# Optimization experiments

Hardware: AMD Instinct MI355X
Metric: run time of the kernel (lower is better)

Reference implementation:

```python
import jax, jax.numpy as jnp
import numpy as np

N_NODES = 50000
N_EDGES = 500000
D_NODE = 128
D_EDGE = 128
HIDDEN = 64


def setup_inputs() -> dict:
    key = jax.random.key(0)
    k = jax.random.split(key, 8)
    x = jax.random.normal(k[0], (N_NODES, D_NODE), dtype=jnp.float32)
    edge_index = jax.random.randint(k[1], (2, N_EDGES), 0, N_NODES, dtype=jnp.int64)
    e = jax.random.normal(k[2], (N_EDGES, D_EDGE), dtype=jnp.float32)
    d_in = 2 * D_NODE + D_EDGE
    # Kaiming-uniform-ish init like torch Linear
    W1 = jax.random.uniform(k[3], (d_in, HIDDEN), jnp.float32, -1.0, 1.0) / np.sqrt(d_in)
    b1 = jax.random.uniform(k[4], (HIDDEN,), jnp.float32, -1.0, 1.0) / np.sqrt(d_in)
    W2 = jax.random.uniform(k[5], (HIDDEN, D_EDGE), jnp.float32, -1.0, 1.0) / np.sqrt(HIDDEN)
    b2 = jax.random.uniform(k[6], (D_EDGE,), jnp.float32, -1.0, 1.0) / np.sqrt(HIDDEN)
    return {"x": x, "edge_index": edge_index, "e": e,
            "W1": W1, "b1": b1, "W2": W2, "b2": b2}


def reference(x, edge_index, e, W1, b1, W2, b2):
    src = edge_index[0]
    dst = edge_index[1]
    # gather node features for each edge endpoint: [E, d_node] each
    inp = jnp.concatenate([x[src], x[dst], e], axis=-1)  # [E, 2*d_node + d_edge]
    h = jax.nn.relu(inp @ W1 + b1)                       # [E, hidden]
    return e + (h @ W2 + b2)                             # residual edge update [E, d_edge]
```

## Files before the change

kernel.cpp:

```cpp
#include <hip/hip_runtime.h>

#define NN   50000
#define EN   500000
#define DN   128
#define DIN  384
#define HID  64
#define NTILES 31250
#define EST  132

typedef __attribute__((ext_vector_type(8))) short bf16x8;
typedef __attribute__((ext_vector_type(4))) float f32x4;

__device__ __forceinline__ short f2bf(float f) {
    union { float f; unsigned u; } v; v.f = f;
    return (short)((v.u + 0x7FFFu + ((v.u >> 16) & 1u)) >> 16);
}

__global__ void prep_weights(const float* __restrict__ W1, const float* __restrict__ W2,
                             short* __restrict__ W1T, short* __restrict__ W2T) {
    int i = blockIdx.x * 256 + threadIdx.x;
    if (i < DIN * HID) {
        int k = i / HID, n = i % HID;
        W1T[n * DIN + k] = f2bf(W1[i]);
    }
    if (i < HID * DN) {
        int k = i / DN, d = i % DN;
        W2T[d * HID + k] = f2bf(W2[i]);
    }
}

__global__ void prep_x(const float* __restrict__ x, short* __restrict__ xb) {
    int i = blockIdx.x * 256 + threadIdx.x;
    if (i >= NN * DN / 8) return;
    const float* p = x + (size_t)i * 8;
    f32x4 v0 = *(const f32x4*)p;
    f32x4 v1 = *(const f32x4*)(p + 4);
    bf16x8 o;
    o[0] = f2bf(v0[0]); o[1] = f2bf(v0[1]); o[2] = f2bf(v0[2]); o[3] = f2bf(v0[3]);
    o[4] = f2bf(v1[0]); o[5] = f2bf(v1[1]); o[6] = f2bf(v1[2]); o[7] = f2bf(v1[3]);
    *(bf16x8*)(xb + (size_t)i * 8) = o;
}

template<bool XB>
__global__ __launch_bounds__(256, 3)
void edge_update(const float* __restrict__ x, const short* __restrict__ xb,
                 const int* __restrict__ ei, const float* __restrict__ e,
                 const float* __restrict__ b1, const float* __restrict__ b2,
                 const short* __restrict__ W1T, const short* __restrict__ W2T,
                 float* __restrict__ out) {
    __shared__ float ebuf[4][16 * EST];
    __shared__ short hbuf[4][16 * 72];

    const int tid  = threadIdx.x;
    const int wave = tid >> 6;
    const int lane = tid & 63;
    const int m    = lane & 15;
    const int q    = lane >> 4;
    const int kq   = q * 8;

    float* eb = &ebuf[wave][0];
    short* hb = &hbuf[wave][0];

    for (int t = 0; t < 2; ++t) {
        const int tile = blockIdx.x * 8 + wave * 2 + t;
        if (tile >= NTILES) continue;
        const int ebase = tile * 16;
        const int edge  = ebase + m;

        const int src = ei[edge];
        const int dst = ei[EN + edge];

        bf16x8 as[4], ad[4], ae[4];
        if (XB) {
            const short* ps = xb + (size_t)src * DN;
            const short* pd = xb + (size_t)dst * DN;
            #pragma unroll
            for (int ks = 0; ks < 4; ++ks) {
                as[ks] = *(const bf16x8*)(ps + ks * 32 + kq);
                ad[ks] = *(const bf16x8*)(pd + ks * 32 + kq);
            }
        } else {
            const float* rs = x + (size_t)src * DN;
            const float* rd = x + (size_t)dst * DN;
            #pragma unroll
            for (int ks = 0; ks < 4; ++ks) {
                f32x4 s0 = *(const f32x4*)(rs + ks * 32 + kq);
                f32x4 s1 = *(const f32x4*)(rs + ks * 32 + kq + 4);
                f32x4 d0 = *(const f32x4*)(rd + ks * 32 + kq);
                f32x4 d1 = *(const f32x4*)(rd + ks * 32 + kq + 4);
                bf16x8 a, b;
                a[0]=f2bf(s0[0]); a[1]=f2bf(s0[1]); a[2]=f2bf(s0[2]); a[3]=f2bf(s0[3]);
                a[4]=f2bf(s1[0]); a[5]=f2bf(s1[1]); a[6]=f2bf(s1[2]); a[7]=f2bf(s1[3]);
                b[0]=f2bf(d0[0]); b[1]=f2bf(d0[1]); b[2]=f2bf(d0[2]); b[3]=f2bf(d0[3]);
                b[4]=f2bf(d1[0]); b[5]=f2bf(d1[1]); b[6]=f2bf(d1[2]); b[7]=f2bf(d1[3]);
                as[ks] = a; ad[ks] = b;
            }
        }

        const float* re = e + (size_t)edge * DN;
        f32x4 ev[8];
        #pragma unroll
        for (int ks = 0; ks < 4; ++ks) {
            ev[2*ks]   = *(const f32x4*)(re + ks * 32 + kq);
            ev[2*ks+1] = *(const f32x4*)(re + ks * 32 + kq + 4);
        }
        #pragma unroll
        for (int ks = 0; ks < 4; ++ks) {
            *(f32x4*)(eb + m * EST + ks * 32 + kq)     = ev[2*ks];
            *(f32x4*)(eb + m * EST + ks * 32 + kq + 4) = ev[2*ks+1];
        }
        #pragma unroll
        for (int ks = 0; ks < 4; ++ks) {
            bf16x8 a;
            a[0]=f2bf(ev[2*ks][0]); a[1]=f2bf(ev[2*ks][1]); a[2]=f2bf(ev[2*ks][2]); a[3]=f2bf(ev[2*ks][3]);
            a[4]=f2bf(ev[2*ks+1][0]); a[5]=f2bf(ev[2*ks+1][1]); a[6]=f2bf(ev[2*ks+1][2]); a[7]=f2bf(ev[2*ks+1][3]);
            ae[ks] = a;
        }

        f32x4 acc1[4];
        #pragma unroll
        for (int nt = 0; nt < 4; ++nt) acc1[nt] = (f32x4){0.f, 0.f, 0.f, 0.f};

        #pragma unroll
        for (int ks = 0; ks < 12; ++ks) {
            bf16x8 a = (ks < 4) ? as[ks] : (ks < 8) ? ad[ks - 4] : ae[ks - 8];
            const int kglob = ks * 32 + kq;
            #pragma unroll
            for (int nt = 0; nt < 4; ++nt) {
                bf16x8 b = *(const bf16x8*)(W1T + (m + 16 * nt) * DIN + kglob);
                acc1[nt] = __builtin_amdgcn_mfma_f32_16x16x32_bf16(a, b, acc1[nt], 0, 0, 0);
            }
        }

        #pragma unroll
        for (int nt = 0; nt < 4; ++nt) {
            const int col = m + 16 * nt;
            const float bv = b1[col];
            #pragma unroll
            for (int r = 0; r < 4; ++r) {
                float h = acc1[nt][r] + bv;
                h = h > 0.f ? h : 0.f;
                hb[(q * 4 + r) * 72 + col] = f2bf(h);
            }
        }

        bf16x8 a0 = *(const bf16x8*)(hb + m * 72 + kq);
        bf16x8 a1 = *(const bf16x8*)(hb + m * 72 + 32 + kq);

        f32x4 acc2[8];
        #pragma unroll
        for (int nt = 0; nt < 8; ++nt) acc2[nt] = (f32x4){0.f, 0.f, 0.f, 0.f};

        #pragma unroll
        for (int nt = 0; nt < 8; ++nt) {
            const short* wp = W2T + (m + 16 * nt) * HID + kq;
            bf16x8 b0  = *(const bf16x8*)wp;
            bf16x8 b1v = *(const bf16x8*)(wp + 32);
            acc2[nt] = __builtin_amdgcn_mfma_f32_16x16x32_bf16(a0, b0,  acc2[nt], 0, 0, 0);
            acc2[nt] = __builtin_amdgcn_mfma_f32_16x16x32_bf16(a1, b1v, acc2[nt], 0, 0, 0);
        }

        #pragma unroll
        for (int nt = 0; nt < 8; ++nt) {
            const int d = m + 16 * nt;
            const float bv = b2[d];
            #pragma unroll
            for (int r = 0; r < 4; ++r) {
                const int row = q * 4 + r;
                out[(size_t)(ebase + row) * DN + d] = eb[row * EST + d] + acc2[nt][r] + bv;
            }
        }
    }
}

extern "C" void kernel_launch(void* const* d_in, const int* in_sizes, int n_in,
                              void* d_out, int out_size, void* d_ws, size_t ws_size,
                              hipStream_t stream) {
    const float* x  = (const float*)d_in[0];
    const int*   ei = (const int*)d_in[1];
    const float* e  = (const float*)d_in[2];
    const float* W1 = (const float*)d_in[3];
    const float* b1 = (const float*)d_in[4];
    const float* W2 = (const float*)d_in[5];
    const float* b2 = (const float*)d_in[6];
    float* out = (float*)d_out;

    short* W1T = (short*)d_ws;
    short* W2T = W1T + HID * DIN;
    short* xb  = W2T + HID * DN;
    const size_t need_xb = (size_t)(HID * DIN + HID * DN + NN * DN) * 2;

    prep_weights<<<96, 256, 0, stream>>>(W1, W2, W1T, W2T);

    const int nblocks = (NTILES + 7) / 8;
    if (ws_size >= need_xb) {
        prep_x<<<(NN * DN / 8 + 255) / 256, 256, 0, stream>>>(x, xb);
        edge_update<true><<<nblocks, 256, 0, stream>>>(x, xb, ei, e, b1, b2, W1T, W2T, out);
    } else {
        edge_update<false><<<nblocks, 256, 0, stream>>>(x, xb, ei, e, b1, b2, W1T, W2T, out);
    }
}
```

Before: 671.8 us.

## Swap second GEMM operands to emit row-contiguous output, drop LDS edge buffer

The second MFMA now has its operands swapped, so each lane holds 4 contiguous output columns of one edge row. That allows vectorized float4 residual reads of e and nontemporal float4 stores instead of scattered scalar stores. The shared-memory staging of e is removed and e is re-read from global (likely L2-resident) for the residual. Edge indices are prefetched for both tiles, and launch bounds are raised to 4 blocks per CU for occupancy, at the risk of register pressure.

```diff
diff --git a/kernel.cpp b/kernel.cpp
--- a/kernel.cpp
+++ b/kernel.cpp
@@ -6,7 +6,6 @@
 #define DIN  384
 #define HID  64
 #define NTILES 31250
-#define EST  132
 
 typedef __attribute__((ext_vector_type(8))) short bf16x8;
 typedef __attribute__((ext_vector_type(4))) float f32x4;
@@ -42,13 +41,12 @@
 }
 
 template<bool XB>
-__global__ __launch_bounds__(256, 3)
+__global__ __launch_bounds__(256, 4)
 void edge_update(const float* __restrict__ x, const short* __restrict__ xb,
                  const int* __restrict__ ei, const float* __restrict__ e,
                  const float* __restrict__ b1, const float* __restrict__ b2,
                  const short* __restrict__ W1T, const short* __restrict__ W2T,
                  float* __restrict__ out) {
-    __shared__ float ebuf[4][16 * EST];
     __shared__ short hbuf[4][16 * 72];
 
     const int tid  = threadIdx.x;
@@ -58,17 +56,26 @@
     const int q    = lane >> 4;
     const int kq   = q * 8;
 
-    float* eb = &ebuf[wave][0];
     short* hb = &hbuf[wave][0];
 
+    int srcs[2], dsts[2];
+    #pragma unroll
+    for (int t = 0; t < 2; ++t) {
+        const int tile = blockIdx.x * 8 + wave * 2 + t;
+        if (tile < NTILES) {
+            const int edge = tile * 16 + m;
+            srcs[t] = ei[edge];
+            dsts[t] = ei[EN + edge];
+        } else { srcs[t] = 0; dsts[t] = 0; }
+    }
+
+    #pragma unroll
     for (int t = 0; t < 2; ++t) {
         const int tile = blockIdx.x * 8 + wave * 2 + t;
         if (tile >= NTILES) continue;
         const int ebase = tile * 16;
-        const int edge  = ebase + m;
-
-        const int src = ei[edge];
-        const int dst = ei[EN + edge];
+        const int src = srcs[t];
+        const int dst = dsts[t];
 
         bf16x8 as[4], ad[4], ae[4];
         if (XB) {
@@ -97,24 +104,21 @@
             }
         }
 
-        const float* re = e + (size_t)edge * DN;
-        f32x4 ev[8];
-        #pragma unroll
-        for (int ks = 0; ks < 4; ++ks) {
-            ev[2*ks]   = *(const f32x4*)(re + ks * 32 + kq);
-            ev[2*ks+1] = *(const f32x4*)(re + ks * 32 + kq + 4);
-        }
-        #pragma unroll
-        for (int ks = 0; ks < 4; ++ks) {
-            *(f32x4*)(eb + m * EST + ks * 32 + kq)     = ev[2*ks];
-            *(f32x4*)(eb + m * EST + ks * 32 + kq + 4) = ev[2*ks+1];
-        }
-        #pragma unroll
-        for (int ks = 0; ks < 4; ++ks) {
-            bf16x8 a;
-            a[0]=f2bf(ev[2*ks][0]); a[1]=f2bf(ev[2*ks][1]); a[2]=f2bf(ev[2*ks][2]); a[3]=f2bf(ev[2*ks][3]);
-            a[4]=f2bf(ev[2*ks+1][0]); a[5]=f2bf(ev[2*ks+1][1]); a[6]=f2bf(ev[2*ks+1][2]); a[7]=f2bf(ev[2*ks+1][3]);
-            ae[ks] = a;
+        {
+            const float* re = e + (size_t)(ebase + m) * DN;
+            f32x4 ev[8];
+            #pragma unroll
+            for (int ks = 0; ks < 4; ++ks) {
+                ev[2*ks]   = *(const f32x4*)(re + ks * 32 + kq);
+                ev[2*ks+1] = *(const f32x4*)(re + ks * 32 + kq + 4);
+            }
+            #pragma unroll
+            for (int ks = 0; ks < 4; ++ks) {
+                bf16x8 a;
+                a[0]=f2bf(ev[2*ks][0]); a[1]=f2bf(ev[2*ks][1]); a[2]=f2bf(ev[2*ks][2]); a[3]=f2bf(ev[2*ks][3]);
+                a[4]=f2bf(ev[2*ks+1][0]); a[5]=f2bf(ev[2*ks+1][1]); a[6]=f2bf(ev[2*ks+1][2]); a[7]=f2bf(ev[2*ks+1][3]);
+                ae[ks] = a;
+            }
         }
 
         f32x4 acc1[4];
@@ -144,8 +148,8 @@
             }
         }
 
-        bf16x8 a0 = *(const bf16x8*)(hb + m * 72 + kq);
-        bf16x8 a1 = *(const bf16x8*)(hb + m * 72 + 32 + kq);
+        bf16x8 ha0 = *(const bf16x8*)(hb + m * 72 + kq);
+        bf16x8 ha1 = *(const bf16x8*)(hb + m * 72 + 32 + kq);
 
         f32x4 acc2[8];
         #pragma unroll
@@ -156,18 +160,19 @@
             const short* wp = W2T + (m + 16 * nt) * HID + kq;
             bf16x8 b0  = *(const bf16x8*)wp;
             bf16x8 b1v = *(const bf16x8*)(wp + 32);
-            acc2[nt] = __builtin_amdgcn_mfma_f32_16x16x32_bf16(a0, b0,  acc2[nt], 0, 0, 0);
-            acc2[nt] = __builtin_amdgcn_mfma_f32_16x16x32_bf16(a1, b1v, acc2[nt], 0, 0, 0);
-        }
-
-        #pragma unroll
-        for (int nt = 0; nt < 8; ++nt) {
-            const int d = m + 16 * nt;
-            const float bv = b2[d];
-            #pragma unroll
-            for (int r = 0; r < 4; ++r) {
-                const int row = q * 4 + r;
-                out[(size_t)(ebase + row) * DN + d] = eb[row * EST + d] + acc2[nt][r] + bv;
+            acc2[nt] = __builtin_amdgcn_mfma_f32_16x16x32_bf16(b0,  ha0, acc2[nt], 0, 0, 0);
+            acc2[nt] = __builtin_amdgcn_mfma_f32_16x16x32_bf16(b1v, ha1, acc2[nt], 0, 0, 0);
+        }
+
+        {
+            const float* er   = e   + (size_t)(ebase + m) * DN + q * 4;
+            float*       orow = out + (size_t)(ebase + m) * DN + q * 4;
+            #pragma unroll
+            for (int nt = 0; nt < 8; ++nt) {
+                f32x4 evv = *(const f32x4*)(er + nt * 16);
+                f32x4 bv  = *(const f32x4*)(b2 + nt * 16 + q * 4);
+                f32x4 o = evv + acc2[nt] + bv;
+                __builtin_nontemporal_store(o, (f32x4*)(orow + nt * 16));
             }
         }
     }
```

After: 717.1 us. 6.7% more time.

## Prefetch both tiles' gathers upfront and vectorize output stores via transposed MFMA

Applied to the files above, without the earlier changes.

Each wave now issues the index, node-feature gather and edge-row loads for both of its tiles before any compute, so the second tile's memory latency overlaps the first tile's MFMA work. The second GEMM swaps its operands so each lane holds four consecutive output columns, which allows 16-byte vectorized residual reads and output stores in place of scalar ones. The b1 bias loads are also hoisted. The cost is higher register pressure, which could reduce occupancy under the 3-waves launch bound.

```diff
diff --git a/kernel.cpp b/kernel.cpp
--- a/kernel.cpp
+++ b/kernel.cpp
@@ -41,6 +41,69 @@
     *(bf16x8*)(xb + (size_t)i * 8) = o;
 }
 
+__device__ __forceinline__ void tile_main(
+    int tile, bool valid, int m, int q, int kq,
+    const bf16x8* as, const bf16x8* ad, const bf16x8* ae,
+    const float* bb1, float* eb, short* hb,
+    const short* __restrict__ W1T, const short* __restrict__ W2T,
+    const float* __restrict__ b2, float* __restrict__ out)
+{
+    if (!valid) return;
+    const int ebase = tile * 16;
+
+    f32x4 acc1[4];
+    #pragma unroll
+    for (int nt = 0; nt < 4; ++nt) acc1[nt] = (f32x4){0.f, 0.f, 0.f, 0.f};
+
+    #pragma unroll
+    for (int ks = 0; ks < 12; ++ks) {
+        bf16x8 a = (ks < 4) ? as[ks] : (ks < 8) ? ad[ks - 4] : ae[ks - 8];
+        const int kglob = ks * 32 + kq;
+        #pragma unroll
+        for (int nt = 0; nt < 4; ++nt) {
+            bf16x8 b = *(const bf16x8*)(W1T + (m + 16 * nt) * DIN + kglob);
+            acc1[nt] = __builtin_amdgcn_mfma_f32_16x16x32_bf16(a, b, acc1[nt], 0, 0, 0);
+        }
+    }
+
+    #pragma unroll
+    for (int nt = 0; nt < 4; ++nt) {
+        const int col = m + 16 * nt;
+        const float bv = bb1[nt];
+        #pragma unroll
+        for (int r = 0; r < 4; ++r) {
+            float h = acc1[nt][r] + bv;
+            h = h > 0.f ? h : 0.f;
+            hb[(q * 4 + r) * 72 + col] = f2bf(h);
+        }
+    }
+
+    bf16x8 ha0 = *(const bf16x8*)(hb + m * 72 + kq);
+    bf16x8 ha1 = *(const bf16x8*)(hb + m * 72 + 32 + kq);
+
+    f32x4 acc2[8];
+    #pragma unroll
+    for (int nt = 0; nt < 8; ++nt) acc2[nt] = (f32x4){0.f, 0.f, 0.f, 0.f};
+
+    #pragma unroll
+    for (int nt = 0; nt < 8; ++nt) {
+        const short* wp = W2T + (m + 16 * nt) * HID + kq;
+        bf16x8 b0  = *(const bf16x8*)wp;
+        bf16x8 b1v = *(const bf16x8*)(wp + 32);
+        acc2[nt] = __builtin_amdgcn_mfma_f32_16x16x32_bf16(b0,  ha0, acc2[nt], 0, 0, 0);
+        acc2[nt] = __builtin_amdgcn_mfma_f32_16x16x32_bf16(b1v, ha1, acc2[nt], 0, 0, 0);
+    }
+
+    const float* ebr  = eb  + m * EST + q * 4;
+    float*       orow = out + (size_t)(ebase + m) * DN + q * 4;
+    #pragma unroll
+    for (int nt = 0; nt < 8; ++nt) {
+        f32x4 evv = *(const f32x4*)(ebr + nt * 16);
+        f32x4 bv  = *(const f32x4*)(b2 + nt * 16 + q * 4);
+        *(f32x4*)(orow + nt * 16) = evv + acc2[nt] + bv;
+    }
+}
+
 template<bool XB>
 __global__ __launch_bounds__(256, 3)
 void edge_update(const float* __restrict__ x, const short* __restrict__ xb,
@@ -61,43 +124,71 @@
     float* eb = &ebuf[wave][0];
     short* hb = &hbuf[wave][0];
 
-    for (int t = 0; t < 2; ++t) {
-        const int tile = blockIdx.x * 8 + wave * 2 + t;
-        if (tile >= NTILES) continue;
-        const int ebase = tile * 16;
-        const int edge  = ebase + m;
-
-        const int src = ei[edge];
-        const int dst = ei[EN + edge];
-
-        bf16x8 as[4], ad[4], ae[4];
-        if (XB) {
-            const short* ps = xb + (size_t)src * DN;
-            const short* pd = xb + (size_t)dst * DN;
-            #pragma unroll
-            for (int ks = 0; ks < 4; ++ks) {
-                as[ks] = *(const bf16x8*)(ps + ks * 32 + kq);
-                ad[ks] = *(const bf16x8*)(pd + ks * 32 + kq);
-            }
-        } else {
-            const float* rs = x + (size_t)src * DN;
-            const float* rd = x + (size_t)dst * DN;
-            #pragma unroll
-            for (int ks = 0; ks < 4; ++ks) {
-                f32x4 s0 = *(const f32x4*)(rs + ks * 32 + kq);
-                f32x4 s1 = *(const f32x4*)(rs + ks * 32 + kq + 4);
-                f32x4 d0 = *(const f32x4*)(rd + ks * 32 + kq);
-                f32x4 d1 = *(const f32x4*)(rd + ks * 32 + kq + 4);
-                bf16x8 a, b;
-                a[0]=f2bf(s0[0]); a[1]=f2bf(s0[1]); a[2]=f2bf(s0[2]); a[3]=f2bf(s0[3]);
-                a[4]=f2bf(s1[0]); a[5]=f2bf(s1[1]); a[6]=f2bf(s1[2]); a[7]=f2bf(s1[3]);
-                b[0]=f2bf(d0[0]); b[1]=f2bf(d0[1]); b[2]=f2bf(d0[2]); b[3]=f2bf(d0[3]);
-                b[4]=f2bf(d1[0]); b[5]=f2bf(d1[1]); b[6]=f2bf(d1[2]); b[7]=f2bf(d1[3]);
-                as[ks] = a; ad[ks] = b;
-            }
-        }
-
-        const float* re = e + (size_t)edge * DN;
+    const int tile0 = blockIdx.x * 8 + wave * 2;
+    const int tile1 = tile0 + 1;
+    const bool v0 = (tile0 < NTILES);
+    const bool v1 = (tile1 < NTILES);
+
+    int src0 = 0, dst0 = 0, src1 = 0, dst1 = 0;
+    if (v0) { src0 = ei[tile0 * 16 + m]; dst0 = ei[EN + tile0 * 16 + m]; }
+    if (v1) { src1 = ei[tile1 * 16 + m]; dst1 = ei[EN + tile1 * 16 + m]; }
+
+    float bb1[4];
+    #pragma unroll
+    for (int nt = 0; nt < 4; ++nt) bb1[nt] = b1[m + 16 * nt];
+
+    bf16x8 as0[4], ad0[4], as1[4], ad1[4];
+    if (XB) {
+        const short* ps0 = xb + (size_t)src0 * DN;
+        const short* pd0 = xb + (size_t)dst0 * DN;
+        const short* ps1 = xb + (size_t)src1 * DN;
+        const short* pd1 = xb + (size_t)dst1 * DN;
+        #pragma unroll
+        for (int ks = 0; ks < 4; ++ks) {
+            as0[ks] = *(const bf16x8*)(ps0 + ks * 32 + kq);
+            ad0[ks] = *(const bf16x8*)(pd0 + ks * 32 + kq);
+        }
+        #pragma unroll
+        for (int ks = 0; ks < 4; ++ks) {
+            as1[ks] = *(const bf16x8*)(ps1 + ks * 32 + kq);
+            ad1[ks] = *(const bf16x8*)(pd1 + ks * 32 + kq);
+        }
+    } else {
+        const float* rs0 = x + (size_t)src0 * DN;
+        const float* rd0 = x + (size_t)dst0 * DN;
+        const float* rs1 = x + (size_t)src1 * DN;
+        const float* rd1 = x + (size_t)dst1 * DN;
+        #pragma unroll
+        for (int ks = 0; ks < 4; ++ks) {
+            f32x4 s0 = *(const f32x4*)(rs0 + ks * 32 + kq);
+            f32x4 s1 = *(const f32x4*)(rs0 + ks * 32 + kq + 4);
+            f32x4 d0 = *(const f32x4*)(rd0 + ks * 32 + kq);
+            f32x4 d1 = *(const f32x4*)(rd0 + ks * 32 + kq + 4);
+            bf16x8 a, b;
+            a[0]=f2bf(s0[0]); a[1]=f2bf(s0[1]); a[2]=f2bf(s0[2]); a[3]=f2bf(s0[3]);
+            a[4]=f2bf(s1[0]); a[5]=f2bf(s1[1]); a[6]=f2bf(s1[2]); a[7]=f2bf(s1[3]);
+            b[0]=f2bf(d0[0]); b[1]=f2bf(d0[1]); b[2]=f2bf(d0[2]); b[3]=f2bf(d0[3]);
+            b[4]=f2bf(d1[0]); b[5]=f2bf(d1[1]); b[6]=f2bf(d1[2]); b[7]=f2bf(d1[3]);
+            as0[ks] = a; ad0[ks] = b;
+        }
+        #pragma unroll
+        for (int ks = 0; ks < 4; ++ks) {
+            f32x4 s0 = *(const f32x4*)(rs1 + ks * 32 + kq);
+            f32x4 s1 = *(const f32x4*)(rs1 + ks * 32 + kq + 4);
+            f32x4 d0 = *(const f32x4*)(rd1 + ks * 32 + kq);
+            f32x4 d1 = *(const f32x4*)(rd1 + ks * 32 + kq + 4);
+            bf16x8 a, b;
+            a[0]=f2bf(s0[0]); a[1]=f2bf(s0[1]); a[2]=f2bf(s0[2]); a[3]=f2bf(s0[3]);
+            a[4]=f2bf(s1[0]); a[5]=f2bf(s1[1]); a[6]=f2bf(s1[2]); a[7]=f2bf(s1[3]);
+            b[0]=f2bf(d0[0]); b[1]=f2bf(d0[1]); b[2]=f2bf(d0[2]); b[3]=f2bf(d0[3]);
+            b[4]=f2bf(d1[0]); b[5]=f2bf(d1[1]); b[6]=f2bf(d1[2]); b[7]=f2bf(d1[3]);
+            as1[ks] = a; ad1[ks] = b;
+        }
+    }
+
+    bf16x8 ae0[4];
+    if (v0) {
+        const float* re = e + (size_t)(tile0 * 16 + m) * DN;
         f32x4 ev[8];
         #pragma unroll
         for (int ks = 0; ks < 4; ++ks) {
@@ -108,69 +199,38 @@
         for (int ks = 0; ks < 4; ++ks) {
             *(f32x4*)(eb + m * EST + ks * 32 + kq)     = ev[2*ks];
             *(f32x4*)(eb + m * EST + ks * 32 + kq + 4) = ev[2*ks+1];
-        }
-        #pragma unroll
-        for (int ks = 0; ks < 4; ++ks) {
             bf16x8 a;
-            a[0]=f2bf(ev[2*ks][0]); a[1]=f2bf(ev[2*ks][1]); a[2]=f2bf(ev[2*ks][2]); a[3]=f2bf(ev[2*ks][3]);
+            a[0]=f2bf(ev[2*ks][0]);   a[1]=f2bf(ev[2*ks][1]);   a[2]=f2bf(ev[2*ks][2]);   a[3]=f2bf(ev[2*ks][3]);
             a[4]=f2bf(ev[2*ks+1][0]); a[5]=f2bf(ev[2*ks+1][1]); a[6]=f2bf(ev[2*ks+1][2]); a[7]=f2bf(ev[2*ks+1][3]);
-            ae[ks] = a;
-        }
-
-        f32x4 acc1[4];
-        #pragma unroll
-        for (int nt = 0; nt < 4; ++nt) acc1[nt] = (f32x4){0.f, 0.f, 0.f, 0.f};
-
-        #pragma unroll
-        for (int ks = 0; ks < 12; ++ks) {
-            bf16x8 a = (ks < 4) ? as[ks] : (ks < 8) ? ad[ks - 4] : ae[ks - 8];
-            const int kglob = ks * 32 + kq;
-            #pragma unroll
-            for (int nt = 0; nt < 4; ++nt) {
-                bf16x8 b = *(const bf16x8*)(W1T + (m + 16 * nt) * DIN + kglob);
-                acc1[nt] = __builtin_amdgcn_mfma_f32_16x16x32_bf16(a, b, acc1[nt], 0, 0, 0);
-            }
-        }
-
-        #pragma unroll
-        for (int nt = 0; nt < 4; ++nt) {
-            const int col = m + 16 * nt;
-            const float bv = b1[col];
-            #pragma unroll
-            for (int r = 0; r < 4; ++r) {
-                float h = acc1[nt][r] + bv;
-                h = h > 0.f ? h : 0.f;
-                hb[(q * 4 + r) * 72 + col] = f2bf(h);
-            }
-        }
-
-        bf16x8 a0 = *(const bf16x8*)(hb + m * 72 + kq);
-        bf16x8 a1 = *(const bf16x8*)(hb + m * 72 + 32 + kq);
-
-        f32x4 acc2[8];
-        #pragma unroll
-        for (int nt = 0; nt < 8; ++nt) acc2[nt] = (f32x4){0.f, 0.f, 0.f, 0.f};
-
-        #pragma unroll
-        for (int nt = 0; nt < 8; ++nt) {
-            const short* wp = W2T + (m + 16 * nt) * HID + kq;
-            bf16x8 b0  = *(const bf16x8*)wp;
-            bf16x8 b1v = *(const bf16x8*)(wp + 32);
-            acc2[nt] = __builtin_amdgcn_mfma_f32_16x16x32_bf16(a0, b0,  acc2[nt], 0, 0, 0);
-            acc2[nt] = __builtin_amdgcn_mfma_f32_16x16x32_bf16(a1, b1v, acc2[nt], 0, 0, 0);
-        }
-
-        #pragma unroll
-        for (int nt = 0; nt < 8; ++nt) {
-            const int d = m + 16 * nt;
-            const float bv = b2[d];
-            #pragma unroll
-            for (int r = 0; r < 4; ++r) {
-                const int row = q * 4 + r;
-                out[(size_t)(ebase + row) * DN + d] = eb[row * EST + d] + acc2[nt][r] + bv;
-            }
-        }
-    }
+            ae0[ks] = a;
+        }
+    }
+
+    f32x4 ev1[8];
+    if (v1) {
+        const float* re = e + (size_t)(tile1 * 16 + m) * DN;
+        #pragma unroll
+        for (int ks = 0; ks < 4; ++ks) {
+            ev1[2*ks]   = *(const f32x4*)(re + ks * 32 + kq);
+            ev1[2*ks+1] = *(const f32x4*)(re + ks * 32 + kq + 4);
+        }
+    }
+
+    tile_main(tile0, v0, m, q, kq, as0, ad0, ae0, bb1, eb, hb, W1T, W2T, b2, out);
+
+    bf16x8 ae1[4];
+    if (v1) {
+        #pragma unroll
+        for (int ks = 0; ks < 4; ++ks) {
+            *(f32x4*)(eb + m * EST + ks * 32 + kq)     = ev1[2*ks];
+            *(f32x4*)(eb + m * EST + ks * 32 + kq + 4) = ev1[2*ks+1];
+            bf16x8 a;
+            a[0]=f2bf(ev1[2*ks][0]);   a[1]=f2bf(ev1[2*ks][1]);   a[2]=f2bf(ev1[2*ks][2]);   a[3]=f2bf(ev1[2*ks][3]);
+            a[4]=f2bf(ev1[2*ks+1][0]); a[5]=f2bf(ev1[2*ks+1][1]); a[6]=f2bf(ev1[2*ks+1][2]); a[7]=f2bf(ev1[2*ks+1][3]);
+            ae1[ks] = a;
+        }
+    }
+    tile_main(tile1, v1, m, q, kq, as1, ad1, ae1, bb1, eb, hb, W1T, W2T, b2, out);
 }
 
 extern "C" void kernel_launch(void* const* d_in, const int* in_sizes, int n_in,
```

Result: no change. 662.8 us (-1.3%).
